# Optimization experiments

Hardware: AMD Instinct MI355X
Metric: run time of the kernel (lower is better)

The kernel has to match this reference:

```python
import jax, jax.numpy as jnp
import numpy as np

HIDDEN = 1024
HEADS = 16
HEAD_DIM = HIDDEN // HEADS


def setup_inputs() -> dict:
    key = jax.random.key(0)
    ks = jax.random.split(key, 11)
    s = 1.0 / np.sqrt(HIDDEN)
    return {
        "query": jax.random.normal(ks[0], (8, 1024, HIDDEN), dtype=jnp.float32),
        "key": jax.random.normal(ks[1], (8, 1024, HIDDEN), dtype=jnp.float32),
        "value": jax.random.normal(ks[2], (8, 1024, HIDDEN), dtype=jnp.float32),
        "Wq": jax.random.uniform(ks[3], (HIDDEN, HIDDEN), jnp.float32, -s, s),
        "bq": jax.random.uniform(ks[4], (HIDDEN,), jnp.float32, -s, s),
        "Wk": jax.random.uniform(ks[5], (HIDDEN, HIDDEN), jnp.float32, -s, s),
        "bk": jax.random.uniform(ks[6], (HIDDEN,), jnp.float32, -s, s),
        "Wv": jax.random.uniform(ks[7], (HIDDEN, HIDDEN), jnp.float32, -s, s),
        "bv": jax.random.uniform(ks[8], (HIDDEN,), jnp.float32, -s, s),
        "Wo": jax.random.uniform(ks[9], (HIDDEN, HIDDEN), jnp.float32, -s, s),
        "bo": jax.random.uniform(ks[10], (HIDDEN,), jnp.float32, -s, s),
    }


def reference(query, key, value, Wq, bq, Wk, bk, Wv, bv, Wo, bo):
    B, S, D = key.shape
    scale = jnp.sqrt(jnp.asarray(HEAD_DIM, dtype=query.dtype))
    # linear projections (torch Linear: x @ W.T + b), split into heads -> [B,H,S,hd]
    def proj(x, W, b):
        return (x @ W.T + b).reshape(B, -1, HEADS, HEAD_DIM).transpose(0, 2, 1, 3)
    q = proj(query, Wq, bq)
    k = proj(key, Wk, bk)
    v = proj(value, Wv, bv)
    # [B,H,Sq,Sk] full attention scores (module materializes them)
    energy = jnp.einsum("bhqd,bhkd->bhqk", q, k) / scale
    attention = jax.nn.softmax(energy, axis=-1)
    # dropout p=0.0 -> identity
    x = jnp.einsum("bhqk,bhkd->bhqd", attention, v)
    x = x.transpose(0, 2, 1, 3).reshape(B, -1, D)
    return x @ Wo.T + bo
```

## Files before the change

### kernel.cpp

```cpp
#include <hip/hip_runtime.h>
#include <hip/hip_bf16.h>
#include <stdint.h>

#define HIDDEN 1024
#define HEADS 16
#define HD 64
#define BATCH 8
#define SEQ 1024
#define MTOT (BATCH*SEQ)

typedef __attribute__((ext_vector_type(4))) float  f32x4;
typedef __attribute__((ext_vector_type(4))) float  float4v;
typedef __attribute__((ext_vector_type(8))) short  s16x8;
typedef __attribute__((ext_vector_type(4))) short  s16x4;
typedef __attribute__((ext_vector_type(4))) unsigned int u32x4;
typedef __bf16 bf16x8 __attribute__((ext_vector_type(8)));

#define QSCALE 0.18033688011112042f

__device__ __forceinline__ short f2bf(float f) {
  uint32_t u = __builtin_bit_cast(uint32_t, f);
  u += 0x7FFFu + ((u >> 16) & 1u);
  return (short)(u >> 16);
}
__device__ __forceinline__ bf16x8 asbf(s16x8 v) {
  return __builtin_bit_cast(bf16x8, v);
}

__device__ __forceinline__ float dpp_fmax16(float x) {
  int t;
  t = __builtin_amdgcn_update_dpp(0, __builtin_bit_cast(int, x), 0xB1, 0xF, 0xF, true);
  x = fmaxf(x, __builtin_bit_cast(float, t));
  t = __builtin_amdgcn_update_dpp(0, __builtin_bit_cast(int, x), 0x4E, 0xF, 0xF, true);
  x = fmaxf(x, __builtin_bit_cast(float, t));
  t = __builtin_amdgcn_update_dpp(0, __builtin_bit_cast(int, x), 0x141, 0xF, 0xF, true);
  x = fmaxf(x, __builtin_bit_cast(float, t));
  t = __builtin_amdgcn_update_dpp(0, __builtin_bit_cast(int, x), 0x140, 0xF, 0xF, true);
  x = fmaxf(x, __builtin_bit_cast(float, t));
  return x;
}
__device__ __forceinline__ float dpp_fadd16(float x) {
  int t;
  t = __builtin_amdgcn_update_dpp(0, __builtin_bit_cast(int, x), 0xB1, 0xF, 0xF, true);
  x += __builtin_bit_cast(float, t);
  t = __builtin_amdgcn_update_dpp(0, __builtin_bit_cast(int, x), 0x4E, 0xF, 0xF, true);
  x += __builtin_bit_cast(float, t);
  t = __builtin_amdgcn_update_dpp(0, __builtin_bit_cast(int, x), 0x141, 0xF, 0xF, true);
  x += __builtin_bit_cast(float, t);
  t = __builtin_amdgcn_update_dpp(0, __builtin_bit_cast(int, x), 0x140, 0xF, 0xF, true);
  x += __builtin_bit_cast(float, t);
  return x;
}

typedef const __attribute__((address_space(1))) void* gvp;
typedef __attribute__((address_space(3)))       void* lvp;
__device__ __forceinline__ void gl_lds16(const void* g, const void* ldsbase) {
  __builtin_amdgcn_global_load_lds((gvp)(uintptr_t)g,
                                   (lvp)(uintptr_t)(uint32_t)(uintptr_t)ldsbase,
                                   16, 0, 0);
}

__global__ __launch_bounds__(256) void cvt_x(const float* __restrict__ src,
                                             short* __restrict__ dst) {
  int i = blockIdx.x * 256 + threadIdx.x;
  float4v a = *(const float4v*)(src + (size_t)i * 8);
  float4v b = *(const float4v*)(src + (size_t)i * 8 + 4);
  s16x8 o = { f2bf(a.x), f2bf(a.y), f2bf(a.z), f2bf(a.w),
              f2bf(b.x), f2bf(b.y), f2bf(b.z), f2bf(b.w) };
  *(s16x8*)(dst + (size_t)i * 8) = o;
}

__global__ __launch_bounds__(256) void cvt_w(const float* __restrict__ s0,
                                             const float* __restrict__ s1,
                                             const float* __restrict__ s2,
                                             const float* __restrict__ s3,
                                             short* __restrict__ dst) {
  int z = blockIdx.y;
  const float* src = (z == 0) ? s0 : (z == 1) ? s1 : (z == 2) ? s2 : s3;
  int i = blockIdx.x * 256 + threadIdx.x;
  float4v a = *(const float4v*)(src + (size_t)i * 8);
  float4v b = *(const float4v*)(src + (size_t)i * 8 + 4);
  s16x8 o = { f2bf(a.x), f2bf(a.y), f2bf(a.z), f2bf(a.w),
              f2bf(b.x), f2bf(b.y), f2bf(b.z), f2bf(b.w) };
  *(s16x8*)(dst + (size_t)z * 1048576 + (size_t)i * 8) = o;
}

__global__ __launch_bounds__(256) void vtrans(const short* __restrict__ Vb,
                                              short* __restrict__ Vt) {
  __shared__ short lt[64 * 64];
  const int t = threadIdx.x;
  const int kt0 = blockIdx.x, h = blockIdx.y, b = blockIdx.z;
  const short* src = Vb + ((size_t)(b * 1024 + kt0 * 64)) * 1024 + h * 64;

  #pragma unroll
  for (int i = 0; i < 2; i++) {
    int c = t + i * 256;
    int s = c >> 3, dc = c & 7;
    s16x8 v = *(const s16x8*)(src + (size_t)s * 1024 + dc * 8);
    int dcp = dc ^ (s & 7) ^ ((s >> 3) & 7);
    *(s16x8*)(&lt[s * 64 + dcp * 8]) = v;
  }
  __syncthreads();

  short* dst = Vt + ((size_t)(b * 16 + h) * 64) * 1024 + kt0 * 64;
  #pragma unroll
  for (int i = 0; i < 2; i++) {
    int c = t + i * 256;
    int d = c >> 3, kc = c & 7;
    s16x8 o;
    #pragma unroll
    for (int j = 0; j < 8; j++) {
      int s = kc * 8 + j;
      o[j] = lt[s * 64 + (((d >> 3) ^ j ^ kc) * 8) + (d & 7)];
    }
    *(s16x8*)(dst + (size_t)d * 1024 + (kc ^ (d & 7)) * 8) = o;
  }
}

template<int CMODE>
__global__ __launch_bounds__(256, 2) void gemm_bf16_dma(
    const short* __restrict__ A, const short* __restrict__ Wb,
    const float* __restrict__ bias, void* __restrict__ Cv, float scale)
{
  __shared__ short Alds[128 * 32];
  __shared__ short Blds[128 * 32];

  const int t  = threadIdx.x;
  const int w  = t >> 6, l = t & 63, g = l >> 4, ln = l & 15;
  const int wr = w >> 1, wc = w & 1;
  const int m0 = blockIdx.x * 128, n0 = blockIdx.y * 128;

  f32x4 acc[4][4];
  #pragma unroll
  for (int i = 0; i < 4; i++)
    #pragma unroll
    for (int j = 0; j < 4; j++) acc[i][j] = (f32x4)0.0f;

  for (int k0 = 0; k0 < 1024; k0 += 32) {
    #pragma unroll
    for (int i = 0; i < 2; i++) {
      int c = i * 256 + w * 64 + l;
      int row = c >> 2, col8 = c & 3;
      gl_lds16(A  + (size_t)(m0 + row) * 1024 + k0 + col8 * 8,
               &Alds[(i * 256 + w * 64) * 8]);
      gl_lds16(Wb + (size_t)(n0 + row) * 1024 + k0 + col8 * 8,
               &Blds[(i * 256 + w * 64) * 8]);
    }
    __syncthreads();

    s16x8 af[4], bfr[4];
    #pragma unroll
    for (int mf = 0; mf < 4; mf++)
      af[mf] = *(const s16x8*)(&Alds[(wr * 64 + mf * 16 + ln) * 32 + g * 8]);
    #pragma unroll
    for (int nf = 0; nf < 4; nf++)
      bfr[nf] = *(const s16x8*)(&Blds[(wc * 64 + nf * 16 + ln) * 32 + g * 8]);

    __builtin_amdgcn_s_setprio(1);
    #pragma unroll
    for (int mf = 0; mf < 4; mf++)
      #pragma unroll
      for (int nf = 0; nf < 4; nf++)
        acc[mf][nf] = __builtin_amdgcn_mfma_f32_16x16x32_bf16(
            asbf(af[mf]), asbf(bfr[nf]), acc[mf][nf], 0, 0, 0);
    __builtin_amdgcn_s_setprio(0);
    __syncthreads();
  }

  float bv[4];
  #pragma unroll
  for (int nf = 0; nf < 4; nf++) bv[nf] = bias[n0 + wc * 64 + nf * 16 + ln];
  #pragma unroll
  for (int mf = 0; mf < 4; mf++)
    #pragma unroll
    for (int nf = 0; nf < 4; nf++)
      #pragma unroll
      for (int r = 0; r < 4; r++) {
        float vv = (acc[mf][nf][r] + bv[nf]) * scale;
        size_t idx = (size_t)(m0 + wr * 64 + mf * 16 + g * 4 + r) * 1024
                   + n0 + wc * 64 + nf * 16 + ln;
        if constexpr (CMODE == 0) ((float*)Cv)[idx] = vv;
        else if constexpr (CMODE == 1) ((short*)Cv)[idx] = f2bf(vv);
        else {
          size_t idxs = idx ^ (size_t)(((g * 4 + r) & 7) * 8);
          ((short*)Cv)[idxs] = f2bf(vv);
        }
      }
}

template<bool A_IS_BF16, bool OUT_IS_F32>
__global__ __launch_bounds__(256, 2) void gemm_bt_bias(
    const void* __restrict__ Av, const float* __restrict__ W,
    const float* __restrict__ bias, void* __restrict__ Cv, float scale)
{
  __shared__ short Alds[128 * 32];
  __shared__ short Blds[128 * 32];

  const int t  = threadIdx.x;
  const int w  = t >> 6, l = t & 63, g = l >> 4, ln = l & 15;
  const int wr = w >> 1, wc = w & 1;
  const int m0 = blockIdx.x * 128, n0 = blockIdx.y * 128;

  f32x4 acc[4][4];
  #pragma unroll
  for (int i = 0; i < 4; i++)
    #pragma unroll
    for (int j = 0; j < 4; j++) acc[i][j] = (f32x4)0.0f;

  const float* Af = (const float*)Av;
  const short* Ab = (const short*)Av;

  for (int k0 = 0; k0 < 1024; k0 += 32) {
    if constexpr (!A_IS_BF16) {
      #pragma unroll
      for (int i = 0; i < 4; i++) {
        int c = i * 256 + t;
        int row = c >> 3, c4 = c & 7;
        float4v v = *(const float4v*)(Af + (size_t)(m0 + row) * 1024 + k0 + c4 * 4);
        s16x4 p = { f2bf(v.x), f2bf(v.y), f2bf(v.z), f2bf(v.w) };
        *(s16x4*)(&Alds[row * 32 + c4 * 4]) = p;
      }
    } else {
      #pragma unroll
      for (int i = 0; i < 2; i++) {
        int c = i * 256 + t;
        int row = c >> 2, c8 = c & 3;
        *(s16x8*)(&Alds[row * 32 + c8 * 8]) =
            *(const s16x8*)(Ab + (size_t)(m0 + row) * 1024 + k0 + c8 * 8);
      }
    }
    #pragma unroll
    for (int i = 0; i < 4; i++) {
      int c = i * 256 + t;
      int row = c >> 3, c4 = c & 7;
      float4v v = *(const float4v*)(W + (size_t)(n0 + row) * 1024 + k0 + c4 * 4);
      s16x4 p = { f2bf(v.x), f2bf(v.y), f2bf(v.z), f2bf(v.w) };
      *(s16x4*)(&Blds[row * 32 + c4 * 4]) = p;
    }
    __syncthreads();

    s16x8 af[4], bfr[4];
    #pragma unroll
    for (int mf = 0; mf < 4; mf++)
      af[mf] = *(const s16x8*)(&Alds[(wr * 64 + mf * 16 + ln) * 32 + g * 8]);
    #pragma unroll
    for (int nf = 0; nf < 4; nf++)
      bfr[nf] = *(const s16x8*)(&Blds[(wc * 64 + nf * 16 + ln) * 32 + g * 8]);

    #pragma unroll
    for (int mf = 0; mf < 4; mf++)
      #pragma unroll
      for (int nf = 0; nf < 4; nf++)
        acc[mf][nf] = __builtin_amdgcn_mfma_f32_16x16x32_bf16(
            asbf(af[mf]), asbf(bfr[nf]), acc[mf][nf], 0, 0, 0);
    __syncthreads();
  }

  float bv[4];
  #pragma unroll
  for (int nf = 0; nf < 4; nf++) bv[nf] = bias[n0 + wc * 64 + nf * 16 + ln];
  #pragma unroll
  for (int mf = 0; mf < 4; mf++)
    #pragma unroll
    for (int nf = 0; nf < 4; nf++)
      #pragma unroll
      for (int r = 0; r < 4; r++) {
        float vv = (acc[mf][nf][r] + bv[nf]) * scale;
        size_t idx = (size_t)(m0 + wr * 64 + mf * 16 + g * 4 + r) * 1024
                   + n0 + wc * 64 + nf * 16 + ln;
        if constexpr (OUT_IS_F32) ((float*)Cv)[idx] = vv;
        else                      ((short*)Cv)[idx] = f2bf(vv);
      }
}

__global__ __launch_bounds__(256, 2) void flash_attn(
    const short* __restrict__ Q, const short* __restrict__ Kswz,
    const short* __restrict__ Vt, short* __restrict__ CTX)
{
  __shared__ short Klds[2][64 * 64];
  __shared__ short Vlds[2][64 * 64];

  const int t  = threadIdx.x;
  const int w  = t >> 6, l = t & 63, g = l >> 4, ln = l & 15;
  const int rb0 = g & 1, rb1 = g >> 1;
  const bool sendK = (rb0 ^ rb1) != 0;
  const int bh   = blockIdx.x & 127;
  const int tile = blockIdx.x >> 7;
  const int b = bh >> 4, h = bh & 15;
  const size_t rowbase = (size_t)b * SEQ;
  const int colbase = h * HD;
  const int q0w = tile * 128 + w * 32;

  const short* Kg = Kswz + rowbase * 1024 + colbase;
  const short* Vg = Vt + (size_t)bh * 65536;
  const int c0 = w * 64 + l;

  const short one_bf = (short)0x3F80;
  const s16x8 ones = { one_bf, one_bf, one_bf, one_bf,
                       one_bf, one_bf, one_bf, one_bf };

  s16x8 qf[2][2];
  #pragma unroll
  for (int mf = 0; mf < 2; mf++)
    #pragma unroll
    for (int kf = 0; kf < 2; kf++)
      qf[mf][kf] = *(const s16x8*)(Q + (rowbase + q0w + mf * 16 + ln) * 1024
                                     + colbase + kf * 32 + g * 8);

  f32x4 acc_o[2][4];
  f32x4 l_acc[2];
  #pragma unroll
  for (int i = 0; i < 2; i++) {
    l_acc[i] = (f32x4)0.0f;
    #pragma unroll
    for (int j = 0; j < 4; j++) acc_o[i][j] = (f32x4)0.0f;
  }

  float m_run[2] = { -1e30f, -1e30f };

  auto STAGE = [&](int buf, int nt) {
    #pragma unroll
    for (int i = 0; i < 2; i++) {
      int c = c0 + i * 256;
      gl_lds16(Kg + (size_t)(nt * 64 + (c >> 3)) * 1024 + (c & 7) * 8,
               &Klds[buf][(i * 256 + w * 64) * 8]);
      gl_lds16(Vg + (size_t)(c >> 3) * 1024 + nt * 64 + (c & 7) * 8,
               &Vlds[buf][(i * 256 + w * 64) * 8]);
    }
  };

  STAGE(0, 0);
  __syncthreads();

  int cur = 0;
  for (int kt = 0; kt < 16; kt++) {
    if (kt < 15) STAGE(cur ^ 1, kt + 1);

    const short* Kc = &Klds[cur][0];
    const short* Vc = &Vlds[cur][0];

    f32x4 sT[4][2];
    #pragma unroll
    for (int i = 0; i < 4; i++)
      #pragma unroll
      for (int j = 0; j < 2; j++) sT[i][j] = (f32x4)0.0f;

    __builtin_amdgcn_s_setprio(1);
    #pragma unroll
    for (int kf = 0; kf < 2; kf++) {
      s16x8 kfr[4];
      #pragma unroll
      for (int nf = 0; nf < 4; nf++)
        kfr[nf] = *(const s16x8*)(Kc + (nf * 16 + ln) * 64
                                     + (((kf * 4 + g) ^ (ln & 7)) * 8));
      #pragma unroll
      for (int kk4 = 0; kk4 < 4; kk4++)
        #pragma unroll
        for (int kq = 0; kq < 2; kq++)
          sT[kk4][kq] = __builtin_amdgcn_mfma_f32_16x16x32_bf16(
              asbf(kfr[kk4]), asbf(qf[kq][kf]), sT[kk4][kq], 0, 0, 0);
    }
    __builtin_amdgcn_s_setprio(0);

    float rm[2];
    #pragma unroll
    for (int kq = 0; kq < 2; kq++) {
      float a0 = fmaxf(sT[0][kq][0], sT[0][kq][1]);
      float a1 = fmaxf(sT[0][kq][2], sT[0][kq][3]);
      float a2 = fmaxf(sT[1][kq][0], sT[1][kq][1]);
      float a3 = fmaxf(sT[1][kq][2], sT[1][kq][3]);
      float a4 = fmaxf(sT[2][kq][0], sT[2][kq][1]);
      float a5 = fmaxf(sT[2][kq][2], sT[2][kq][3]);
      float a6 = fmaxf(sT[3][kq][0], sT[3][kq][1]);
      float a7 = fmaxf(sT[3][kq][2], sT[3][kq][3]);
      float b0 = fmaxf(a0, a1), b1 = fmaxf(a2, a3);
      float b2 = fmaxf(a4, a5), b3 = fmaxf(a6, a7);
      float mx = fmaxf(fmaxf(b0, b1), fmaxf(b2, b3));
      mx = fmaxf(mx, __shfl_xor(mx, 16));
      mx = fmaxf(mx, __shfl_xor(mx, 32));
      rm[kq] = mx;
    }
    float worst = fmaxf(rm[0] - m_run[0], rm[1] - m_run[1]);

    if (__all(worst <= 8.0f)) {
      #pragma unroll
      for (int kq = 0; kq < 2; kq++) {
        float m0v = m_run[kq];
        #pragma unroll
        for (int kk4 = 0; kk4 < 4; kk4++)
          #pragma unroll
          for (int r = 0; r < 4; r++)
            sT[kk4][kq][r] = exp2f(sT[kk4][kq][r] - m0v);
      }
    } else {
      float sc[2];
      #pragma unroll
      for (int kq = 0; kq < 2; kq++) {
        float mnew = fmaxf(m_run[kq], rm[kq]);
        sc[kq] = exp2f(m_run[kq] - mnew);
        m_run[kq] = mnew;
        #pragma unroll
        for (int kk4 = 0; kk4 < 4; kk4++)
          #pragma unroll
          for (int r = 0; r < 4; r++)
            sT[kk4][kq][r] = exp2f(sT[kk4][kq][r] - mnew);
      }
      #pragma unroll
      for (int mf = 0; mf < 2; mf++)
        #pragma unroll
        for (int r = 0; r < 4; r++) {
          float scr = __shfl(sc[mf], g * 4 + r);
          l_acc[mf][r] *= scr;
          #pragma unroll
          for (int nf = 0; nf < 4; nf++) acc_o[mf][nf][r] *= scr;
        }
    }

    uint32_t D[4][2][2];
    #pragma unroll
    for (int kk4 = 0; kk4 < 4; kk4++)
      #pragma unroll
      for (int kq = 0; kq < 2; kq++) {
        asm("v_cvt_pk_bf16_f32 %0, %1, %2"
            : "=v"(D[kk4][kq][0]) : "v"(sT[kk4][kq][0]), "v"(sT[kk4][kq][1]));
        asm("v_cvt_pk_bf16_f32 %0, %1, %2"
            : "=v"(D[kk4][kq][1]) : "v"(sT[kk4][kq][2]), "v"(sT[kk4][kq][3]));
      }

    s16x8 pa[2][2];
    #pragma unroll
    for (int kq = 0; kq < 2; kq++)
      #pragma unroll
      for (int kp = 0; kp < 2; kp++) {
        uint32_t K0 = rb1 ? D[2*kp+1][kq][0] : D[2*kp][kq][0];
        uint32_t K1 = rb1 ? D[2*kp+1][kq][1] : D[2*kp][kq][1];
        uint32_t S0 = rb1 ? D[2*kp][kq][0]   : D[2*kp+1][kq][0];
        uint32_t S1 = rb1 ? D[2*kp][kq][1]   : D[2*kp+1][kq][1];
        uint32_t R0 = (uint32_t)__shfl_xor((int)S0, 32);
        uint32_t R1 = (uint32_t)__shfl_xor((int)S1, 32);
        uint32_t T0 = sendK ? K0 : R0, T1 = sendK ? K1 : R1;
        uint32_t V0 = sendK ? R0 : K0, V1 = sendK ? R1 : K1;
        uint32_t U0 = (uint32_t)__shfl_xor((int)T0, 16);
        uint32_t U1 = (uint32_t)__shfl_xor((int)T1, 16);
        u32x4 dw = { rb0 ? U0 : V0, rb0 ? U1 : V1,
                     rb0 ? V0 : U0, rb0 ? V1 : U1 };
        pa[kq][kp] = __builtin_bit_cast(s16x8, dw);
      }

    s16x8 vbf[4][2];
    #pragma unroll
    for (int nf = 0; nf < 4; nf++)
      #pragma unroll
      for (int kf = 0; kf < 2; kf++)
        vbf[nf][kf] = *(const s16x8*)(Vc + (nf * 16 + ln) * 64
                                         + (((kf * 4 + g) ^ (ln & 7)) * 8));

    __builtin_amdgcn_s_setprio(1);
    #pragma unroll
    for (int kf = 0; kf < 2; kf++)
      #pragma unroll
      for (int mf = 0; mf < 2; mf++) {
        l_acc[mf] = __builtin_amdgcn_mfma_f32_16x16x32_bf16(
            asbf(pa[mf][kf]), asbf(ones), l_acc[mf], 0, 0, 0);
        #pragma unroll
        for (int nf = 0; nf < 4; nf++)
          acc_o[mf][nf] = __builtin_amdgcn_mfma_f32_16x16x32_bf16(
              asbf(pa[mf][kf]), asbf(vbf[nf][kf]), acc_o[mf][nf], 0, 0, 0);
      }
    __builtin_amdgcn_s_setprio(0);

    __syncthreads();
    cur ^= 1;
  }

  #pragma unroll
  for (int mf = 0; mf < 2; mf++)
    #pragma unroll
    for (int r = 0; r < 4; r++) {
      float inv = 1.0f / l_acc[mf][r];
      size_t row = rowbase + q0w + mf * 16 + g * 4 + r;
      #pragma unroll
      for (int nf = 0; nf < 4; nf++)
        CTX[row * 1024 + colbase + nf * 16 + ln] = f2bf(acc_o[mf][nf][r] * inv);
    }
}

__global__ __launch_bounds__(256, 2) void flash_attn_fb(
    const short* __restrict__ Q, const short* __restrict__ K,
    const short* __restrict__ V, short* __restrict__ CTX)
{
  __shared__ short Klds[2][64 * 64];
  __shared__ short Vtl [2][64 * 64];
  __shared__ short Plds[4][32 * 72];

  const int t  = threadIdx.x;
  const int w  = t >> 6, l = t & 63, g = l >> 4, ln = l & 15;
  const int tile = blockIdx.x & 7;
  const int bh   = blockIdx.x >> 3;
  const int b = bh >> 4, h = bh & 15;
  const size_t rowbase = (size_t)b * SEQ;
  const int colbase = h * HD;
  const int q0w = tile * 128 + w * 32;

  const int kk0  = t >> 3;
  const int dblk = t & 7;
  const int ksw  = (dblk ^ (kk0 & 7)) * 8;
  const int kWr  = kk0 * 64 + dblk * 8;
  const short* Kg = K + rowbase * 1024 + colbase + ksw;
  const short* Vg = V + rowbase * 1024 + colbase + dblk * 8;

  s16x8 qf[2][2];
  #pragma unroll
  for (int mf = 0; mf < 2; mf++)
    #pragma unroll
    for (int kf = 0; kf < 2; kf++)
      qf[mf][kf] = *(const s16x8*)(Q + (rowbase + q0w + mf * 16 + ln) * 1024
                                     + colbase + kf * 32 + g * 8);

  f32x4 acc_o[2][4];
  #pragma unroll
  for (int i = 0; i < 2; i++)
    #pragma unroll
    for (int j = 0; j < 4; j++) acc_o[i][j] = (f32x4)0.0f;

  float m_run[2][4], l_run[2][4];
  #pragma unroll
  for (int i = 0; i < 2; i++)
    #pragma unroll
    for (int r = 0; r < 4; r++) { m_run[i][r] = -1e30f; l_run[i][r] = 0.0f; }

  auto storeKV = [&](int buf, s16x8 ka, s16x8 kb, s16x8 va, s16x8 vb8) {
    short* Kd = &Klds[buf][0];
    short* Vd = &Vtl[buf][0];
    *(s16x8*)(Kd + kWr)        = ka;
    *(s16x8*)(Kd + kWr + 2048) = kb;
    #pragma unroll
    for (int e = 0; e < 8; e++) {
      int a0 = (dblk * 8 + e) * 64 + (kk0 ^ ((e ^ dblk) * 8));
      Vd[a0]      = va[e];
      Vd[a0 ^ 32] = vb8[e];
    }
  };

  s16x8 kvA = *(const s16x8*)(Kg + (size_t)kk0 * 1024);
  s16x8 kvB = *(const s16x8*)(Kg + (size_t)(kk0 + 32) * 1024);
  s16x8 vvA = *(const s16x8*)(Vg + (size_t)kk0 * 1024);
  s16x8 vvB = *(const s16x8*)(Vg + (size_t)(kk0 + 32) * 1024);
  storeKV(0, kvA, kvB, vvA, vvB);

  int cur = 0;
  for (int kt = 0; kt < 16; kt++) {
    if (kt < 15) {
      const size_t r0 = (size_t)((kt + 1) * 64 + kk0) * 1024;
      kvA = *(const s16x8*)(Kg + r0);
      kvB = *(const s16x8*)(Kg + r0 + 32 * 1024);
      vvA = *(const s16x8*)(Vg + r0);
      vvB = *(const s16x8*)(Vg + r0 + 32 * 1024);
    }
    __syncthreads();

    const short* Kc = &Klds[cur][0];
    const short* Vc = &Vtl[cur][0];

    f32x4 s_acc[2][4];
    #pragma unroll
    for (int i = 0; i < 2; i++)
      #pragma unroll
      for (int j = 0; j < 4; j++) s_acc[i][j] = (f32x4)0.0f;

    #pragma unroll
    for (int kf = 0; kf < 2; kf++) {
      s16x8 kfr[4];
      #pragma unroll
      for (int nf = 0; nf < 4; nf++)
        kfr[nf] = *(const s16x8*)(Kc + (nf * 16 + ln) * 64
                                     + (((kf * 4 + g) ^ (ln & 7)) * 8));
      #pragma unroll
      for (int mf = 0; mf < 2; mf++)
        #pragma unroll
        for (int nf = 0; nf < 4; nf++)
          s_acc[mf][nf] = __builtin_amdgcn_mfma_f32_16x16x32_bf16(
              asbf(qf[mf][kf]), asbf(kfr[nf]), s_acc[mf][nf], 0, 0, 0);
    }

    float smax[2][4];
    float worst = -1e30f;
    #pragma unroll
    for (int mf = 0; mf < 2; mf++)
      #pragma unroll
      for (int r = 0; r < 4; r++) {
        float mx = fmaxf(fmaxf(s_acc[mf][0][r], s_acc[mf][1][r]),
                         fmaxf(s_acc[mf][2][r], s_acc[mf][3][r]));
        mx = dpp_fmax16(mx);
        smax[mf][r] = mx;
        worst = fmaxf(worst, mx - m_run[mf][r]);
      }

    if (__all(worst <= 8.0f)) {
      #pragma unroll
      for (int mf = 0; mf < 2; mf++)
        #pragma unroll
        for (int r = 0; r < 4; r++) {
          float m0v = m_run[mf][r];
          float rs = 0.0f;
          #pragma unroll
          for (int nf = 0; nf < 4; nf++) {
            float pv = exp2f(s_acc[mf][nf][r] - m0v);
            s_acc[mf][nf][r] = pv;
            rs += pv;
          }
          l_run[mf][r] += rs;
        }
    } else {
      #pragma unroll
      for (int mf = 0; mf < 2; mf++)
        #pragma unroll
        for (int r = 0; r < 4; r++) {
          float mnew = fmaxf(m_run[mf][r], smax[mf][r]);
          float sc = exp2f(m_run[mf][r] - mnew);
          m_run[mf][r] = mnew;
          float rs = 0.0f;
          #pragma unroll
          for (int nf = 0; nf < 4; nf++) {
            float pv = exp2f(s_acc[mf][nf][r] - mnew);
            s_acc[mf][nf][r] = pv;
            rs += pv;
          }
          l_run[mf][r] = l_run[mf][r] * sc + rs;
          #pragma unroll
          for (int nf = 0; nf < 4; nf++) acc_o[mf][nf][r] *= sc;
        }
    }

    short* Pw = &Plds[w][0];
    #pragma unroll
    for (int mf = 0; mf < 2; mf++)
      #pragma unroll
      for (int nf = 0; nf < 4; nf++) {
        uint32_t p01, p23;
        asm("v_cvt_pk_bf16_f32 %0, %1, %2"
            : "=v"(p01) : "v"(s_acc[mf][nf][0]), "v"(s_acc[mf][nf][1]));
        asm("v_cvt_pk_bf16_f32 %0, %1, %2"
            : "=v"(p23) : "v"(s_acc[mf][nf][2]), "v"(s_acc[mf][nf][3]));
        int pb = (mf * 16 + g * 4) * 72 + ((nf * 16 + ln) ^ (g << 3));
        Pw[pb]       = (short)p01;
        Pw[pb + 72]  = (short)(p01 >> 16);
        Pw[pb + 144] = (short)p23;
        Pw[pb + 216] = (short)(p23 >> 16);
      }

    s16x8 pa[2][2], vbf[4][2];
    #pragma unroll
    for (int mf = 0; mf < 2; mf++)
      #pragma unroll
      for (int kf = 0; kf < 2; kf++)
        pa[mf][kf] = *(const s16x8*)(
            &Pw[(mf * 16 + ln) * 72 + (((kf * 4 + g) ^ (ln >> 2)) << 3)]);
    #pragma unroll
    for (int nf = 0; nf < 4; nf++)
      #pragma unroll
      for (int kf = 0; kf < 2; kf++) {
        int d  = nf * 16 + ln;
        int sw = (d & 7) ^ (d >> 3);
        vbf[nf][kf] = *(const s16x8*)(Vc + d * 64 + ((kf * 32 + g * 8) ^ (sw * 8)));
      }

    #pragma unroll
    for (int kf = 0; kf < 2; kf++)
      #pragma unroll
      for (int mf = 0; mf < 2; mf++)
        #pragma unroll
        for (int nf = 0; nf < 4; nf++)
          acc_o[mf][nf] = __builtin_amdgcn_mfma_f32_16x16x32_bf16(
              asbf(pa[mf][kf]), asbf(vbf[nf][kf]), acc_o[mf][nf], 0, 0, 0);

    if (kt < 15) {
      storeKV(cur ^ 1, kvA, kvB, vvA, vvB);
      cur ^= 1;
    }
  }

  #pragma unroll
  for (int mf = 0; mf < 2; mf++)
    #pragma unroll
    for (int r = 0; r < 4; r++) {
      float inv = 1.0f / dpp_fadd16(l_run[mf][r]);
      size_t row = rowbase + q0w + mf * 16 + g * 4 + r;
      #pragma unroll
      for (int nf = 0; nf < 4; nf++)
        CTX[row * 1024 + colbase + nf * 16 + ln] = f2bf(acc_o[mf][nf][r] * inv);
    }
}

extern "C" void kernel_launch(void* const* d_in, const int* in_sizes, int n_in,
                              void* d_out, int out_size, void* d_ws, size_t ws_size,
                              hipStream_t stream) {
  const float* query = (const float*)d_in[0];
  const float* key   = (const float*)d_in[1];
  const float* value = (const float*)d_in[2];
  const float* Wq = (const float*)d_in[3];
  const float* bq = (const float*)d_in[4];
  const float* Wk = (const float*)d_in[5];
  const float* bk = (const float*)d_in[6];
  const float* Wv = (const float*)d_in[7];
  const float* bv = (const float*)d_in[8];
  const float* Wo = (const float*)d_in[9];
  const float* bo = (const float*)d_in[10];

  const size_t E = (size_t)MTOT * 1024;
  short* Qb = (short*)d_ws;
  short* Kb = Qb + E;
  short* Vb = Kb + E;
  short* Cx = Vb + E;
  short* T  = Cx + E;
  short* Wb = T  + E;

  const size_t need = (5 * E + 4ull * 1048576) * 2;
  dim3 gg(MTOT / 128, HIDDEN / 128), bb(256);
  dim3 fg(BATCH * HEADS * (SEQ / 128));

  if (ws_size >= need) {
    cvt_w<<<dim3(512, 4), bb, 0, stream>>>(Wq, Wk, Wv, Wo, Wb);
    cvt_x<<<4096, bb, 0, stream>>>(query, T);
    gemm_bf16_dma<1><<<gg, bb, 0, stream>>>(T, Wb + 0 * 1048576, bq, Qb, QSCALE);
    cvt_x<<<4096, bb, 0, stream>>>(key, T);
    gemm_bf16_dma<2><<<gg, bb, 0, stream>>>(T, Wb + 1 * 1048576, bk, Kb, 1.0f);
    cvt_x<<<4096, bb, 0, stream>>>(value, T);
    gemm_bf16_dma<1><<<gg, bb, 0, stream>>>(T, Wb + 2 * 1048576, bv, Vb, 1.0f);
    vtrans<<<dim3(16, 16, 8), bb, 0, stream>>>(Vb, T);
    flash_attn<<<fg, bb, 0, stream>>>(Qb, Kb, T, Cx);
    gemm_bf16_dma<0><<<gg, bb, 0, stream>>>(Cx, Wb + 3 * 1048576, bo, (float*)d_out, 1.0f);
  } else {
    gemm_bt_bias<false, false><<<gg, bb, 0, stream>>>(query, Wq, bq, Qb, QSCALE);
    gemm_bt_bias<false, false><<<gg, bb, 0, stream>>>(key,   Wk, bk, Kb, 1.0f);
    gemm_bt_bias<false, false><<<gg, bb, 0, stream>>>(value, Wv, bv, Vb, 1.0f);
    flash_attn_fb<<<fg, bb, 0, stream>>>(Qb, Kb, Vb, Cx);
    gemm_bt_bias<true, true><<<gg, bb, 0, stream>>>(Cx, Wo, bo, (float*)d_out, 1.0f);
  }
}
```

Measured before the change: 221.9 us.

## Batch Q/K/V conversion and projection GEMMs into single grid-z launches

Adds a cvt_x3 kernel that converts query, key and value to bf16 in one launch, and a gemm_qkv kernel that runs all three projection GEMMs as one grid with blockIdx.z choosing the input, weight, bias, scale and output swizzle. This replaces six serialized launches with two larger ones, which is meant to cut launch gaps and the tail underutilization of each smaller GEMM. It needs a larger workspace (three bf16 staging buffers) and keeps the older path as a fallback. The new GEMM issues global-to-LDS loads and MFMAs in the same iteration with two barriers and no double buffering, so it may have less load/compute overlap than the existing gemm_bf16_dma if that kernel overlaps them.

Result: faster. 212.5 us (-4.2%).

```diff
diff --git a/kernel.cpp b/kernel.cpp
--- a/kernel.cpp
+++ b/kernel.cpp
@@ -68,6 +68,20 @@
   s16x8 o = { f2bf(a.x), f2bf(a.y), f2bf(a.z), f2bf(a.w),
               f2bf(b.x), f2bf(b.y), f2bf(b.z), f2bf(b.w) };
   *(s16x8*)(dst + (size_t)i * 8) = o;
+}
+
+__global__ __launch_bounds__(256) void cvt_x3(const float* __restrict__ s0,
+                                              const float* __restrict__ s1,
+                                              const float* __restrict__ s2,
+                                              short* __restrict__ dst) {
+  int z = blockIdx.y;
+  const float* src = (z == 0) ? s0 : (z == 1) ? s1 : s2;
+  int i = blockIdx.x * 256 + threadIdx.x;
+  float4v a = *(const float4v*)(src + (size_t)i * 8);
+  float4v b = *(const float4v*)(src + (size_t)i * 8 + 4);
+  s16x8 o = { f2bf(a.x), f2bf(a.y), f2bf(a.z), f2bf(a.w),
+              f2bf(b.x), f2bf(b.y), f2bf(b.z), f2bf(b.w) };
+  *(s16x8*)(dst + (size_t)z * ((size_t)MTOT * 1024) + (size_t)i * 8) = o;
 }
 
 __global__ __launch_bounds__(256) void cvt_w(const float* __restrict__ s0,
@@ -185,6 +199,83 @@
           size_t idxs = idx ^ (size_t)(((g * 4 + r) & 7) * 8);
           ((short*)Cv)[idxs] = f2bf(vv);
         }
+      }
+}
+
+__global__ __launch_bounds__(256, 2) void gemm_qkv(
+    const short* __restrict__ X3, const short* __restrict__ Wb,
+    const float* __restrict__ bq, const float* __restrict__ bk,
+    const float* __restrict__ bv_, short* __restrict__ Qb,
+    short* __restrict__ Kb, short* __restrict__ Vb)
+{
+  __shared__ short Alds[128 * 32];
+  __shared__ short Blds[128 * 32];
+
+  const size_t E = (size_t)MTOT * 1024;
+  const int z = blockIdx.z;
+  const short* A  = X3 + (size_t)z * E;
+  const short* W  = Wb + (size_t)z * 1048576;
+  const float* bias = (z == 0) ? bq : (z == 1) ? bk : bv_;
+  short* Cv = (z == 0) ? Qb : (z == 1) ? Kb : Vb;
+  const float scale = (z == 0) ? QSCALE : 1.0f;
+  const bool kswz = (z == 1);
+
+  const int t  = threadIdx.x;
+  const int w  = t >> 6, l = t & 63, g = l >> 4, ln = l & 15;
+  const int wr = w >> 1, wc = w & 1;
+  const int m0 = blockIdx.x * 128, n0 = blockIdx.y * 128;
+
+  f32x4 acc[4][4];
+  #pragma unroll
+  for (int i = 0; i < 4; i++)
+    #pragma unroll
+    for (int j = 0; j < 4; j++) acc[i][j] = (f32x4)0.0f;
+
+  for (int k0 = 0; k0 < 1024; k0 += 32) {
+    #pragma unroll
+    for (int i = 0; i < 2; i++) {
+      int c = i * 256 + w * 64 + l;
+      int row = c >> 2, col8 = c & 3;
+      gl_lds16(A + (size_t)(m0 + row) * 1024 + k0 + col8 * 8,
+               &Alds[(i * 256 + w * 64) * 8]);
+      gl_lds16(W + (size_t)(n0 + row) * 1024 + k0 + col8 * 8,
+               &Blds[(i * 256 + w * 64) * 8]);
+    }
+    __syncthreads();
+
+    s16x8 af[4], bfr[4];
+    #pragma unroll
+    for (int mf = 0; mf < 4; mf++)
+      af[mf] = *(const s16x8*)(&Alds[(wr * 64 + mf * 16 + ln) * 32 + g * 8]);
+    #pragma unroll
+    for (int nf = 0; nf < 4; nf++)
+      bfr[nf] = *(const s16x8*)(&Blds[(wc * 64 + nf * 16 + ln) * 32 + g * 8]);
+
+    __builtin_amdgcn_s_setprio(1);
+    #pragma unroll
+    for (int mf = 0; mf < 4; mf++)
+      #pragma unroll
+      for (int nf = 0; nf < 4; nf++)
+        acc[mf][nf] = __builtin_amdgcn_mfma_f32_16x16x32_bf16(
+            asbf(af[mf]), asbf(bfr[nf]), acc[mf][nf], 0, 0, 0);
+    __builtin_amdgcn_s_setprio(0);
+    __syncthreads();
+  }
+
+  float bv[4];
+  #pragma unroll
+  for (int nf = 0; nf < 4; nf++) bv[nf] = bias[n0 + wc * 64 + nf * 16 + ln];
+  #pragma unroll
+  for (int mf = 0; mf < 4; mf++)
+    #pragma unroll
+    for (int nf = 0; nf < 4; nf++)
+      #pragma unroll
+      for (int r = 0; r < 4; r++) {
+        float vv = (acc[mf][nf][r] + bv[nf]) * scale;
+        size_t idx = (size_t)(m0 + wr * 64 + mf * 16 + g * 4 + r) * 1024
+                   + n0 + wc * 64 + nf * 16 + ln;
+        if (kswz) idx ^= (size_t)(((g * 4 + r) & 7) * 8);
+        Cv[idx] = f2bf(vv);
       }
 }
 
@@ -708,18 +799,36 @@
   const float* bo = (const float*)d_in[10];
 
   const size_t E = (size_t)MTOT * 1024;
-  short* Qb = (short*)d_ws;
-  short* Kb = Qb + E;
-  short* Vb = Kb + E;
-  short* Cx = Vb + E;
-  short* T  = Cx + E;
-  short* Wb = T  + E;
-
-  const size_t need = (5 * E + 4ull * 1048576) * 2;
+  const size_t need_b = (7 * E + 4ull * 1048576) * 2;
+  const size_t need_s = (5 * E + 4ull * 1048576) * 2;
+
   dim3 gg(MTOT / 128, HIDDEN / 128), bb(256);
   dim3 fg(BATCH * HEADS * (SEQ / 128));
 
-  if (ws_size >= need) {
+  if (ws_size >= need_b) {
+    short* Qb = (short*)d_ws;
+    short* Kb = Qb + E;
+    short* Vb = Kb + E;
+    short* Cx = Vb + E;
+    short* T0 = Cx + E;
+    short* Wb = T0 + 3 * E;
+
+    cvt_w<<<dim3(512, 4), bb, 0, stream>>>(Wq, Wk, Wv, Wo, Wb);
+    cvt_x3<<<dim3(4096, 3), bb, 0, stream>>>(query, key, value, T0);
+    gemm_qkv<<<dim3(MTOT / 128, HIDDEN / 128, 3), bb, 0, stream>>>(
+        T0, Wb, bq, bk, bv, Qb, Kb, Vb);
+    vtrans<<<dim3(16, 16, 8), bb, 0, stream>>>(Vb, T0);
+    flash_attn<<<fg, bb, 0, stream>>>(Qb, Kb, T0, Cx);
+    gemm_bf16_dma<0><<<gg, bb, 0, stream>>>(Cx, Wb + 3 * 1048576, bo,
+                                            (float*)d_out, 1.0f);
+  } else if (ws_size >= need_s) {
+    short* Qb = (short*)d_ws;
+    short* Kb = Qb + E;
+    short* Vb = Kb + E;
+    short* Cx = Vb + E;
+    short* T  = Cx + E;
+    short* Wb = T  + E;
+
     cvt_w<<<dim3(512, 4), bb, 0, stream>>>(Wq, Wk, Wv, Wo, Wb);
     cvt_x<<<4096, bb, 0, stream>>>(query, T);
     gemm_bf16_dma<1><<<gg, bb, 0, stream>>>(T, Wb + 0 * 1048576, bq, Qb, QSCALE);
@@ -729,8 +838,14 @@
     gemm_bf16_dma<1><<<gg, bb, 0, stream>>>(T, Wb + 2 * 1048576, bv, Vb, 1.0f);
     vtrans<<<dim3(16, 16, 8), bb, 0, stream>>>(Vb, T);
     flash_attn<<<fg, bb, 0, stream>>>(Qb, Kb, T, Cx);
-    gemm_bf16_dma<0><<<gg, bb, 0, stream>>>(Cx, Wb + 3 * 1048576, bo, (float*)d_out, 1.0f);
+    gemm_bf16_dma<0><<<gg, bb, 0, stream>>>(Cx, Wb + 3 * 1048576, bo,
+                                            (float*)d_out, 1.0f);
   } else {
+    short* Qb = (short*)d_ws;
+    short* Kb = Qb + E;
+    short* Vb = Kb + E;
+    short* Cx = Vb + E;
+
     gemm_bt_bias<false, false><<<gg, bb, 0, stream>>>(query, Wq, bq, Qb, QSCALE);
     gemm_bt_bias<false, false><<<gg, bb, 0, stream>>>(key,   Wk, bk, Kb, 1.0f);
     gemm_bt_bias<false, false><<<gg, bb, 0, stream>>>(value, Wv, bv, Vb, 1.0f);
```
